# Performance work log

Measured on AMD Instinct MI355X. Metric: run time of the kernel, lower is better.

## Reference

```python
import jax, jax.numpy as jnp
import numpy as np

B, V, C, H, W, D = 1, 3, 32, 320, 320, 32


def setup_inputs() -> dict:
    key = jax.random.key(0)
    ks = jax.random.split(key, 14)
    feats = jax.random.normal(ks[0], (B, V, C, H, W), jnp.float32)
    # Valid pinhole projections: P = [[K @ [R|t]], [0,0,0,1]], identity rotation,
    # horizontal baselines sized so the warp stays mostly in-image over the depth range.
    K = np.array([[400.0, 0.0, W / 2.0], [0.0, 400.0, H / 2.0], [0.0, 0.0, 1.0]])
    mats = []
    for tx in (0.0, 100.0, -100.0):
        Rt = np.eye(4)
        Rt[0, 3] = tx
        P = np.eye(4)
        P[:3, :4] = K @ Rt[:3, :4]
        mats.append(P)
    proj = jnp.asarray(np.broadcast_to(np.stack(mats)[None], (B, V, 4, 4)).copy(), jnp.float32)
    planes = jnp.linspace(425.0, 935.0, D, dtype=jnp.float32)
    depth_values = jnp.broadcast_to(planes[None, :, None, None], (B, D, H, W)).astype(jnp.float32)
    s = 0.05  # small init so exp(reg_cost) stays well-scaled
    W0 = s * jax.random.normal(ks[1], (8, C, 3, 3), jnp.float32)
    Ws1 = s * jax.random.normal(ks[2], (8, 8, 3, 3), jnp.float32)
    W1 = s * jax.random.normal(ks[3], (16, 8, 3, 3), jnp.float32)
    Ws2 = s * jax.random.normal(ks[4], (16, 16, 3, 3), jnp.float32)
    W2 = s * jax.random.normal(ks[5], (32, 16, 3, 3), jnp.float32)
    Ws3 = s * jax.random.normal(ks[6], (32, 32, 3, 3), jnp.float32)
    W3 = s * jax.random.normal(ks[7], (64, 32, 3, 3), jnp.float32)
    Ws4 = s * jax.random.normal(ks[8], (64, 64, 3, 3), jnp.float32)
    U4 = s * jax.random.normal(ks[9], (32, 64, 1, 1), jnp.float32)
    U3 = s * jax.random.normal(ks[10], (16, 32, 1, 1), jnp.float32)
    U2 = s * jax.random.normal(ks[11], (8, 16, 1, 1), jnp.float32)
    Wout = s * jax.random.normal(ks[12], (1, 8, 3, 3), jnp.float32)
    return dict(feats=feats, proj=proj, depth_values=depth_values, W0=W0, Ws1=Ws1,
                W1=W1, Ws2=Ws2, W2=W2, Ws3=Ws3, W3=W3, Ws4=Ws4, U4=U4, U3=U3, U2=U2, Wout=Wout)


def _conv(x, w, stride=1):
    return jax.lax.conv_general_dilated(x, w, (stride, stride), 'SAME',
                                        dimension_numbers=('NCHW', 'OIHW', 'NCHW'))


def _up2(x):
    return jnp.repeat(jnp.repeat(x, 2, axis=2), 2, axis=3)


def _bilinear(img, x, y):
    # img [C,H,W]; x,y [N] pixel coords; zero padding, align_corners semantics
    Cc, Hh, Ww = img.shape
    x0 = jnp.floor(x)
    y0 = jnp.floor(y)
    wx = x - x0
    wy = y - y0

    def tap(xi, yi):
        valid = ((xi >= 0) & (xi <= Ww - 1) & (yi >= 0) & (yi <= Hh - 1)).astype(img.dtype)
        xc = jnp.clip(xi, 0, Ww - 1).astype(jnp.int32)
        yc = jnp.clip(yi, 0, Hh - 1).astype(jnp.int32)
        return img[:, yc, xc] * valid  # [C,N]

    return (tap(x0, y0) * (1 - wx) * (1 - wy) + tap(x0 + 1, y0) * wx * (1 - wy)
            + tap(x0, y0 + 1) * (1 - wx) * wy + tap(x0 + 1, y0 + 1) * wx * wy)


def _forward(feats, proj, depth_values, W0, Ws1, W1, Ws2, W2, Ws3, W3, Ws4, U4, U3, U2, Wout):
    Bn, Vn, Cn, Hn, Wn = feats.shape
    Dn = depth_values.shape[1]
    N = Hn * Wn
    relu = jax.nn.relu
    ref = feats[:, 0]
    ref_sq = ref * ref
    # Precompute per-src-view rotated pixel rays and translations.
    inv_ref = jnp.linalg.inv(proj[:, 0])                       # [B,4,4]
    rel = jnp.einsum('bvij,bjk->bvik', proj[:, 1:], inv_ref)   # [B,V-1,4,4]
    rot, trans = rel[:, :, :3, :3], rel[:, :, :3, 3]
    ys, xs = jnp.meshgrid(jnp.arange(Hn), jnp.arange(Wn), indexing='ij')
    pix = jnp.stack([xs.ravel(), ys.ravel(), jnp.ones(N)], 0).astype(feats.dtype)  # [3,N]
    rot_pix = jnp.einsum('bvij,jn->bvin', rot, pix)            # [B,V-1,3,N]

    def regularize(x, s1, s2, s3, s4):
        c1 = relu(_conv(x, W0) + _conv(s1, Ws1))
        c2 = relu(_conv(c1, W1, 2) + _conv(s2, Ws2))
        c3 = relu(_conv(c2, W2, 2) + _conv(s3, Ws3))
        c4 = relu(_conv(c3, W3, 2) + _conv(s4, Ws4))
        u3 = c3 + _up2(_conv(c4, U4))
        u2 = c2 + _up2(_conv(u3, U3))
        u1 = c1 + _up2(_conv(u2, U2))
        return _conv(u1, Wout), c1, c2, c3, c4

    def step(carry, depth_slice):  # depth_slice [B,H,W]
        s1, s2, s3, s4, exp_sum, depth_img, max_prob = carry
        vol_sum, vol_sq = ref, ref_sq
        dflat = depth_slice.reshape(Bn, 1, N)
        for v in range(Vn - 1):
            xyz = rot_pix[:, v] * dflat + trans[:, v, :, None]   # [B,3,N]
            px = xyz[:, 0] / xyz[:, 2]
            py = xyz[:, 1] / xyz[:, 2]
            warped = jax.vmap(_bilinear)(feats[:, v + 1], px, py).reshape(Bn, Cn, Hn, Wn)
            vol_sum = vol_sum + warped
            vol_sq = vol_sq + warped * warped
        variance = vol_sq / Vn - (vol_sum / Vn) ** 2
        cost, s1, s2, s3, s4 = regularize(variance, s1, s2, s3, s4)
        prob = jnp.exp(cost)                                     # [B,1,H,W]
        max_prob = jnp.maximum(max_prob, prob)                   # == flag*prob + (1-flag)*max
        depth_img = depth_img + depth_slice[:, None] * prob
        exp_sum = exp_sum + prob
        return (s1, s2, s3, s4, exp_sum, depth_img, max_prob), None

    z = lambda c, h, w: jnp.zeros((Bn, c, h, w), feats.dtype)
    init = (z(8, Hn, Wn), z(16, Hn // 2, Wn // 2), z(32, Hn // 4, Wn // 4), z(64, Hn // 8, Wn // 8),
            z(1, Hn, Wn), z(1, Hn, Wn), z(1, Hn, Wn))
    carry, _ = jax.lax.scan(step, init, jnp.moveaxis(depth_values, 1, 0))
    _, _, _, _, exp_sum, depth_img, max_prob = carry
    es = exp_sum + 1e-10
    depth_map = (depth_img / es)[:, 0]
    prob_map = (max_prob / es)[:, 0]
    return jnp.stack([depth_map, prob_map], axis=1)  # [B,2,H,W]


def reference(feats, proj, depth_values, W0, Ws1, W1, Ws2, W2, Ws3, W3, Ws4, U4, U3, U2, Wout):
    return _forward(feats, proj, depth_values, W0, Ws1, W1, Ws2, W2, Ws3, W3, Ws4, U4, U3, U2, Wout)
```

## Files before the change

kernel.cpp:

```cpp
#include <hip/hip_runtime.h>
#include <math.h>

#define HH 320
#define WW 320
#define NP (HH*WW)
#define CC 32
#define DD 32

#define H2 160
#define W2 160
#define N2 (H2*W2)
#define H4 80
#define W4 80
#define N4 (H4*W4)
#define H8 40
#define W8 40
#define N8 (H8*W8)

#define HALO 18
#define NHALO (HALO*HALO)

#define C1SZ (8*NP)
#define C2SZ (16*N2)
#define C3SZ (32*N4)
#define C4SZ (64*N8)

#define SMEM_FLOATS (32*NHALO)

#define OFF_REL   0
#define OFF_C1R   64
#define OFF_C2R   (OFF_C1R + 5*C1SZ)
#define OFF_C3R   (OFF_C2R + 4*C2SZ)
#define OFF_C4R   (OFF_C3R + 3*C3SZ)
#define OFF_ESUM  (OFF_C4R + 2*C4SZ)
#define OFF_DIMG  (OFF_ESUM + NP)
#define OFF_MAXP  (OFF_DIMG + NP)
#define OFF_ACCE  (OFF_MAXP + NP)
#define OFF_FT    OFF_ACCE
#define OFF_END   (OFF_FT + 3*CC*NP)

__global__ void k_prep(const float* __restrict__ proj, float* __restrict__ rel) {
    if (threadIdx.x != 0 || blockIdx.x != 0) return;
    double a[4][8];
    for (int i = 0; i < 4; i++)
        for (int j = 0; j < 4; j++) {
            a[i][j] = (double)proj[i*4 + j];
            a[i][j+4] = (i == j) ? 1.0 : 0.0;
        }
    for (int c = 0; c < 4; c++) {
        int pv = c; double best = fabs(a[c][c]);
        for (int r = c+1; r < 4; r++) {
            double v = fabs(a[r][c]);
            if (v > best) { best = v; pv = r; }
        }
        if (pv != c)
            for (int j = 0; j < 8; j++) { double t = a[c][j]; a[c][j] = a[pv][j]; a[pv][j] = t; }
        double inv = 1.0 / a[c][c];
        for (int j = 0; j < 8; j++) a[c][j] *= inv;
        for (int r = 0; r < 4; r++) if (r != c) {
            double f = a[r][c];
            for (int j = 0; j < 8; j++) a[r][j] -= f * a[c][j];
        }
    }
    for (int v = 1; v < 3; v++) {
        const float* P = proj + v*16;
        double rm[4][4];
        for (int i = 0; i < 4; i++)
            for (int j = 0; j < 4; j++) {
                double s = 0.0;
                for (int k = 0; k < 4; k++) s += (double)P[i*4 + k] * a[k][j+4];
                rm[i][j] = s;
            }
        float* o = rel + (v-1)*12;
        o[0]=(float)rm[0][0]; o[1]=(float)rm[0][1]; o[2]=(float)rm[0][2];
        o[3]=(float)rm[1][0]; o[4]=(float)rm[1][1]; o[5]=(float)rm[1][2];
        o[6]=(float)rm[2][0]; o[7]=(float)rm[2][1]; o[8]=(float)rm[2][2];
        o[9]=(float)rm[0][3]; o[10]=(float)rm[1][3]; o[11]=(float)rm[2][3];
    }
}

__global__ __launch_bounds__(256) void k_transpose(const float* __restrict__ feats,
                                                   float* __restrict__ featsT) {
    __shared__ float lds[32][65];
    int g = blockIdx.x;
    int v = g / 1600;
    int p0 = (g - v*1600) * 64;
    const float* src = feats + (size_t)v*CC*NP + p0;
    for (int i = threadIdx.x; i < 32*64; i += 256) {
        int c = i >> 6, pp = i & 63;
        lds[c][pp] = src[(size_t)c*NP + pp];
    }
    __syncthreads();
    float* dst = featsT + ((size_t)v*NP + p0)*32;
    int pp = threadIdx.x >> 2, cq = (threadIdx.x & 3) * 8;
    float4 o0, o1;
    o0.x = lds[cq+0][pp]; o0.y = lds[cq+1][pp]; o0.z = lds[cq+2][pp]; o0.w = lds[cq+3][pp];
    o1.x = lds[cq+4][pp]; o1.y = lds[cq+5][pp]; o1.z = lds[cq+6][pp]; o1.w = lds[cq+7][pp];
    float* w = dst + pp*32 + cq;
    *(float4*)w = o0;
    *(float4*)(w+4) = o1;
}


__device__ void stageA(int blk, int d, int useT,
        const float* __restrict__ feats, const float* __restrict__ featsT,
        const float* __restrict__ rel,
        const float* __restrict__ depthv, const float* __restrict__ c1r,
        const float* __restrict__ W0, const float* __restrict__ Ws1,
        float* buf) {
    const float* dslice = depthv + (size_t)d * NP;
    const float* s1 = c1r + (size_t)((d+4)%5) * C1SZ;
    float* c1out = (float*)c1r + (size_t)(d%5) * C1SZ;

    int bx = blk % 20, by = blk / 20;
    int ox0 = bx*16, oy0 = by*16;

    const float* f1 = feats + CC*NP;
    const float* f2 = feats + 2*CC*NP;
    const float* fT0 = featsT;
    const float* fT1 = featsT + (size_t)CC*NP;
    const float* fT2 = featsT + (size_t)2*CC*NP;
    const float inv3 = 1.0f / 3.0f;

    int opx = threadIdx.x & 15, opy = threadIdx.x >> 4;
    int obase = opy*HALO + opx;
    int outp = (oy0 + opy)*WW + ox0 + opx;

    for (int s = 0; s < 2; s++) {
        int hp = threadIdx.x + s*256;
        if (hp >= NHALO) break;
        int hy = hp / HALO, hx = hp - hy*HALO;
        int gy = oy0 + hy - 1, gx = ox0 + hx - 1;
        if (gy < 0 || gy >= HH || gx < 0 || gx >= WW) {
#pragma unroll 8
            for (int c = 0; c < 32; c++) buf[c*NHALO + hp] = 0.0f;
            continue;
        }
        int p = gy*WW + gx;
        float depth = dslice[p];
        float fx = (float)gx, fy = (float)gy;
        int offs[8]; float wts[8];
#pragma unroll
        for (int v = 0; v < 2; v++) {
            const float* r = rel + v*12;
            float X = (r[0]*fx + r[1]*fy + r[2]) * depth + r[9];
            float Y = (r[3]*fx + r[4]*fy + r[5]) * depth + r[10];
            float Z = (r[6]*fx + r[7]*fy + r[8]) * depth + r[11];
            float iz = 1.0f / Z;
            float px = X * iz, py = Y * iz;
            float x0f = floorf(px), y0f = floorf(py);
            float wx = px - x0f, wy = py - y0f;
            int x0 = (int)x0f, y0 = (int)y0f;
#pragma unroll
            for (int t = 0; t < 4; t++) {
                int xi = x0 + (t & 1), yi = y0 + (t >> 1);
                float wgt = ((t & 1) ? wx : 1.0f - wx) * ((t >> 1) ? wy : 1.0f - wy);
                bool valid = (xi >= 0) && (xi <= WW-1) && (yi >= 0) && (yi <= HH-1);
                int xc = min(max(xi, 0), WW-1);
                int yc = min(max(yi, 0), HH-1);
                offs[v*4 + t] = yc*WW + xc;
                wts[v*4 + t] = valid ? wgt : 0.0f;
            }
        }

        if (useT) {
            float sum[32], sq[32], t[32];
            {
                const float4* q0 = (const float4*)(fT0 + ((size_t)p << 5));
#pragma unroll
                for (int q = 0; q < 8; q++) {
                    float4 v = q0[q];
                    sum[4*q+0] = v.x; sum[4*q+1] = v.y; sum[4*q+2] = v.z; sum[4*q+3] = v.w;
                }
#pragma unroll
                for (int c = 0; c < 32; c++) sq[c] = sum[c]*sum[c];
            }
#pragma unroll
            for (int c = 0; c < 32; c++) t[c] = 0.0f;
#pragma unroll
            for (int tp = 0; tp < 4; tp++) {
                const float4* q1 = (const float4*)(fT1 + ((size_t)offs[tp] << 5));
                float w = wts[tp];
#pragma unroll
                for (int q = 0; q < 8; q++) {
                    float4 v = q1[q];
                    t[4*q+0] += v.x*w; t[4*q+1] += v.y*w; t[4*q+2] += v.z*w; t[4*q+3] += v.w*w;
                }
            }
#pragma unroll
            for (int c = 0; c < 32; c++) { sum[c] += t[c]; sq[c] += t[c]*t[c]; }
#pragma unroll
            for (int c = 0; c < 32; c++) t[c] = 0.0f;
#pragma unroll
            for (int tp = 0; tp < 4; tp++) {
                const float4* q2 = (const float4*)(fT2 + ((size_t)offs[4+tp] << 5));
                float w = wts[4+tp];
#pragma unroll
                for (int q = 0; q < 8; q++) {
                    float4 v = q2[q];
                    t[4*q+0] += v.x*w; t[4*q+1] += v.y*w; t[4*q+2] += v.z*w; t[4*q+3] += v.w*w;
                }
            }
#pragma unroll
            for (int c = 0; c < 32; c++) { sum[c] += t[c]; sq[c] += t[c]*t[c]; }
#pragma unroll
            for (int c = 0; c < 32; c++) {
                float m = sum[c] * inv3;
                buf[c*NHALO + hp] = sq[c] * inv3 - m*m;
            }
        } else {
            for (int c = 0; c < 32; c++) {
                float rv = feats[c*NP + p];
                const float* b1 = f1 + c*NP;
                float t1 = b1[offs[0]]*wts[0] + b1[offs[1]]*wts[1]
                         + b1[offs[2]]*wts[2] + b1[offs[3]]*wts[3];
                const float* b2 = f2 + c*NP;
                float t2 = b2[offs[4]]*wts[4] + b2[offs[5]]*wts[5]
                         + b2[offs[6]]*wts[6] + b2[offs[7]]*wts[7];
                float sum = rv + t1 + t2;
                float sq  = rv*rv + t1*t1 + t2*t2;
                float m = sum * inv3;
                buf[c*NHALO + hp] = sq * inv3 - m*m;
            }
        }
    }
    __syncthreads();

    float acc[8];
#pragma unroll
    for (int o = 0; o < 8; o++) acc[o] = 0.0f;

    for (int ci = 0; ci < 32; ci++) {
        float t[9];
#pragma unroll
        for (int ky = 0; ky < 3; ky++)
#pragma unroll
            for (int kx = 0; kx < 3; kx++) t[ky*3+kx] = buf[ci*NHALO + obase + ky*HALO + kx];
#pragma unroll
        for (int o = 0; o < 8; o++) {
            const float* w = W0 + (o*32 + ci)*9;
            float a = acc[o];
#pragma unroll
            for (int k = 0; k < 9; k++) a += t[k] * w[k];
            acc[o] = a;
        }
    }
    __syncthreads();

    for (int hp = threadIdx.x; hp < NHALO; hp += 256) {
        int hy = hp / HALO, hx = hp - hy*HALO;
        int gy = oy0 + hy - 1, gx = ox0 + hx - 1;
        bool v = (gy >= 0) && (gy < HH) && (gx >= 0) && (gx < WW);
        int p = v ? gy*WW + gx : 0;
#pragma unroll
        for (int c = 0; c < 8; c++) buf[c*NHALO + hp] = v ? s1[c*NP + p] : 0.0f;
    }
    __syncthreads();
    for (int ci = 0; ci < 8; ci++) {
        float t[9];
#pragma unroll
        for (int ky = 0; ky < 3; ky++)
#pragma unroll
            for (int kx = 0; kx < 3; kx++) t[ky*3+kx] = buf[ci*NHALO + obase + ky*HALO + kx];
#pragma unroll
        for (int o = 0; o < 8; o++) {
            const float* w = Ws1 + (o*8 + ci)*9;
            float a = acc[o];
#pragma unroll
            for (int k = 0; k < 9; k++) a += t[k] * w[k];
            acc[o] = a;
        }
    }
#pragma unroll
    for (int o = 0; o < 8; o++) c1out[o*NP + outp] = fmaxf(acc[o], 0.0f);
}

__device__ void stageB(int blk, int d,
        const float* __restrict__ c1r, const float* __restrict__ c2r_,
        const float* __restrict__ W1, const float* __restrict__ Ws2) {
    const float* c1 = c1r + (size_t)(d%5) * C1SZ;
    const float* s2 = c2r_ + (size_t)((d+3)%4) * C2SZ;
    float* c2 = (float*)c2r_ + (size_t)(d%4) * C2SZ;
    int p = (blk % 100)*256 + threadIdx.x;
    if (p >= N2) return;
    int og = blk / 100;
    int y = p / W2, x = p - y*W2;
    int offsA[9]; float mskA[9];
#pragma unroll
    for (int k = 0; k < 9; k++) {
        int yy = 2*y + k/3, xx = 2*x + k%3;
        bool v = (yy < HH) && (xx < WW);
        offsA[k] = v ? yy*WW + xx : 0;
        mskA[k] = v ? 1.0f : 0.0f;
    }
    int offsB[9]; float mskB[9];
#pragma unroll
    for (int k = 0; k < 9; k++) {
        int yy = y + k/3 - 1, xx = x + k%3 - 1;
        bool v = (yy >= 0) && (yy < H2) && (xx >= 0) && (xx < W2);
        offsB[k] = v ? yy*W2 + xx : 0;
        mskB[k] = v ? 1.0f : 0.0f;
    }
    float acc[4];
#pragma unroll
    for (int o = 0; o < 4; o++) acc[o] = 0.0f;
    for (int ci = 0; ci < 8; ci++) {
        const float* b = c1 + ci*NP;
        float t[9];
#pragma unroll
        for (int k = 0; k < 9; k++) t[k] = b[offsA[k]] * mskA[k];
#pragma unroll
        for (int o = 0; o < 4; o++) {
            const float* w = W1 + ((og*4 + o)*8 + ci)*9;
            float a = acc[o];
#pragma unroll
            for (int k = 0; k < 9; k++) a += t[k] * w[k];
            acc[o] = a;
        }
    }
    for (int ci = 0; ci < 16; ci++) {
        const float* b = s2 + ci*N2;
        float t[9];
#pragma unroll
        for (int k = 0; k < 9; k++) t[k] = b[offsB[k]] * mskB[k];
#pragma unroll
        for (int o = 0; o < 4; o++) {
            const float* w = Ws2 + ((og*4 + o)*16 + ci)*9;
            float a = acc[o];
#pragma unroll
            for (int k = 0; k < 9; k++) a += t[k] * w[k];
            acc[o] = a;
        }
    }
#pragma unroll
    for (int o = 0; o < 4; o++) c2[(og*4 + o)*N2 + p] = fmaxf(acc[o], 0.0f);
}

__device__ void stageC(int blk, int d,
        const float* __restrict__ c2r_, const float* __restrict__ c3r_,
        const float* __restrict__ W2w, const float* __restrict__ Ws3) {
    const float* c2 = c2r_ + (size_t)(d%4) * C2SZ;
    const float* s3 = c3r_ + (size_t)((d+2)%3) * C3SZ;
    float* c3 = (float*)c3r_ + (size_t)(d%3) * C3SZ;
    int p = (blk % 25)*256 + threadIdx.x;
    if (p >= N4) return;
    int og = blk / 25;
    int y = p / W4, x = p - y*W4;
    int offsA[9]; float mskA[9];
#pragma unroll
    for (int k = 0; k < 9; k++) {
        int yy = 2*y + k/3, xx = 2*x + k%3;
        bool v = (yy < H2) && (xx < W2);
        offsA[k] = v ? yy*W2 + xx : 0;
        mskA[k] = v ? 1.0f : 0.0f;
    }
    int offsB[9]; float mskB[9];
#pragma unroll
    for (int k = 0; k < 9; k++) {
        int yy = y + k/3 - 1, xx = x + k%3 - 1;
        bool v = (yy >= 0) && (yy < H4) && (xx >= 0) && (xx < W4);
        offsB[k] = v ? yy*W4 + xx : 0;
        mskB[k] = v ? 1.0f : 0.0f;
    }
    float acc[4];
#pragma unroll
    for (int o = 0; o < 4; o++) acc[o] = 0.0f;
    for (int ci = 0; ci < 16; ci++) {
        const float* b = c2 + ci*N2;
        float t[9];
#pragma unroll
        for (int k = 0; k < 9; k++) t[k] = b[offsA[k]] * mskA[k];
#pragma unroll
        for (int o = 0; o < 4; o++) {
            const float* w = W2w + ((og*4 + o)*16 + ci)*9;
            float a = acc[o];
#pragma unroll
            for (int k = 0; k < 9; k++) a += t[k] * w[k];
            acc[o] = a;
        }
    }
    for (int ci = 0; ci < 32; ci++) {
        const float* b = s3 + ci*N4;
        float t[9];
#pragma unroll
        for (int k = 0; k < 9; k++) t[k] = b[offsB[k]] * mskB[k];
#pragma unroll
        for (int o = 0; o < 4; o++) {
            const float* w = Ws3 + ((og*4 + o)*32 + ci)*9;
            float a = acc[o];
#pragma unroll
            for (int k = 0; k < 9; k++) a += t[k] * w[k];
            acc[o] = a;
        }
    }
#pragma unroll
    for (int o = 0; o < 4; o++) c3[(og*4 + o)*N4 + p] = fmaxf(acc[o], 0.0f);
}

__device__ void stageD(int blk, int d,
        const float* __restrict__ c3r_, const float* __restrict__ c4r_,
        const float* __restrict__ W3w, const float* __restrict__ Ws4) {
    const float* c3 = c3r_ + (size_t)(d%3) * C3SZ;
    const float* s4 = c4r_ + (size_t)((d+1)%2) * C4SZ;
    float* c4 = (float*)c4r_ + (size_t)(d%2) * C4SZ;
    int p = (blk % 7)*256 + threadIdx.x;
    if (p >= N8) return;
    int og = blk / 7;
    int y = p / W8, x = p - y*W8;
    int offsA[9]; float mskA[9];
#pragma unroll
    for (int k = 0; k < 9; k++) {
        int yy = 2*y + k/3, xx = 2*x + k%3;
        bool v = (yy < H4) && (xx < W4);
        offsA[k] = v ? yy*W4 + xx : 0;
        mskA[k] = v ? 1.0f : 0.0f;
    }
    int offsB[9]; float mskB[9];
#pragma unroll
    for (int k = 0; k < 9; k++) {
        int yy = y + k/3 - 1, xx = x + k%3 - 1;
        bool v = (yy >= 0) && (yy < H8) && (xx >= 0) && (xx < W8);
        offsB[k] = v ? yy*W8 + xx : 0;
        mskB[k] = v ? 1.0f : 0.0f;
    }
    float acc[4];
#pragma unroll
    for (int o = 0; o < 4; o++) acc[o] = 0.0f;
    for (int ci = 0; ci < 32; ci++) {
        const float* b = c3 + ci*N4;
        float t[9];
#pragma unroll
        for (int k = 0; k < 9; k++) t[k] = b[offsA[k]] * mskA[k];
#pragma unroll
        for (int o = 0; o < 4; o++) {
            const float* w = W3w + ((og*4 + o)*32 + ci)*9;
            float a = acc[o];
#pragma unroll
            for (int k = 0; k < 9; k++) a += t[k] * w[k];
            acc[o] = a;
        }
    }
    for (int ci = 0; ci < 64; ci++) {
        const float* b = s4 + ci*N8;
        float t[9];
#pragma unroll
        for (int k = 0; k < 9; k++) t[k] = b[offsB[k]] * mskB[k];
#pragma unroll
        for (int o = 0; o < 4; o++) {
            const float* w = Ws4 + ((og*4 + o)*64 + ci)*9;
            float a = acc[o];
#pragma unroll
            for (int k = 0; k < 9; k++) a += t[k] * w[k];
            acc[o] = a;
        }
    }
#pragma unroll
    for (int o = 0; o < 4; o++) c4[(og*4 + o)*N8 + p] = fmaxf(acc[o], 0.0f);
}

__device__ void stageU(int blk, int d,
        const float* __restrict__ c1r, const float* __restrict__ c2r_,
        const float* __restrict__ c3r_, const float* __restrict__ c4r_,
        const float* __restrict__ U4, const float* __restrict__ U3,
        const float* __restrict__ U2, const float* __restrict__ Wout,
        const float* __restrict__ depthv,
        float* __restrict__ exp_sum, float* __restrict__ depth_img,
        float* __restrict__ max_prob, float* smem) {
    const float* c1 = c1r + (size_t)(d%5) * C1SZ;
    const float* c2 = c2r_ + (size_t)(d%4) * C2SZ;
    const float* c3 = c3r_ + (size_t)(d%3) * C3SZ;
    const float* c4 = c4r_ + (size_t)(d%2) * C4SZ;
    const float* dslice = depthv + (size_t)d * NP;
    float* u3s = smem;
    float* u2s = smem + 32*36;
    float* u1s = smem + 32*36 + 16*100;

    int bx = blk % 20, by = blk / 20;
    int ox0 = bx*16, oy0 = by*16;
    int qy0 = (oy0 >> 2) - 1, qx0 = (ox0 >> 2) - 1;
    int hy0 = (oy0 >> 1) - 1, hx0 = (ox0 >> 1) - 1;

    for (int i = threadIdx.x; i < 32*36; i += 256) {
        int ch = i / 36, pp = i - ch*36;
        int y4 = qy0 + pp/6, x4 = qx0 + pp%6;
        int y4c = min(max(y4, 0), H4-1), x4c = min(max(x4, 0), W4-1);
        int pl = (y4c >> 1)*W8 + (x4c >> 1);
        const float* w = U4 + ch*64;
        float s = c3[ch*N4 + y4c*W4 + x4c];
#pragma unroll 8
        for (int ci = 0; ci < 64; ci++) s += c4[ci*N8 + pl] * w[ci];
        u3s[ch*36 + pp] = s;
    }
    __syncthreads();
    for (int i = threadIdx.x; i < 16*100; i += 256) {
        int ch = i / 100, pp = i - ch*100;
        int y2 = hy0 + pp/10, x2 = hx0 + pp%10;
        int y2c = min(max(y2, 0), H2-1), x2c = min(max(x2, 0), W2-1);
        int ly = (y2c >> 1) - qy0, lx = (x2c >> 1) - qx0;
        const float* w = U3 + ch*32;
        float s = c2[ch*N2 + y2c*W2 + x2c];
#pragma unroll 8
        for (int ci = 0; ci < 32; ci++) s += u3s[ci*36 + ly*6 + lx] * w[ci];
        u2s[ch*100 + pp] = s;
    }
    __syncthreads();
    for (int i = threadIdx.x; i < 8*NHALO; i += 256) {
        int ch = i / NHALO, pp = i - ch*NHALO;
        int gy = oy0 + pp/HALO - 1, gx = ox0 + pp%HALO - 1;
        float s = 0.0f;
        if (gy >= 0 && gy < HH && gx >= 0 && gx < WW) {
            int ly = (gy >> 1) - hy0, lx = (gx >> 1) - hx0;
            const float* w = U2 + ch*16;
            s = c1[ch*NP + gy*WW + gx];
#pragma unroll
            for (int ci = 0; ci < 16; ci++) s += u2s[ci*100 + ly*10 + lx] * w[ci];
        }
        u1s[ch*NHALO + pp] = s;
    }
    __syncthreads();
    int px = threadIdx.x & 15, py = threadIdx.x >> 4;
    int base = py*HALO + px;
    float cost = 0.0f;
#pragma unroll
    for (int ci = 0; ci < 8; ci++) {
        const float* w = Wout + ci*9;
#pragma unroll
        for (int ky = 0; ky < 3; ky++)
#pragma unroll
            for (int kx = 0; kx < 3; kx++)
                cost += u1s[ci*NHALO + base + ky*HALO + kx] * w[ky*3 + kx];
    }
    int p = (oy0 + py)*WW + ox0 + px;
    float prob = expf(cost);
    exp_sum[p] += prob;
    depth_img[p] += dslice[p] * prob;
    max_prob[p] = fmaxf(max_prob[p], prob);
}

__global__ __launch_bounds__(256) void k_uber(
        int t, int useT,
        const float* __restrict__ feats, const float* __restrict__ featsT,
        const float* __restrict__ rel,
        const float* __restrict__ depthv,
        const float* __restrict__ W0, const float* __restrict__ Ws1,
        const float* __restrict__ W1, const float* __restrict__ Ws2,
        const float* __restrict__ W2w, const float* __restrict__ Ws3,
        const float* __restrict__ W3w, const float* __restrict__ Ws4,
        const float* __restrict__ U4, const float* __restrict__ U3,
        const float* __restrict__ U2, const float* __restrict__ Wout,
        float* __restrict__ c1r, float* __restrict__ c2r,
        float* __restrict__ c3r, float* __restrict__ c4r,
        float* __restrict__ esum, float* __restrict__ dimg,
        float* __restrict__ maxp) {
    __shared__ float smem[SMEM_FLOATS];
    int b = blockIdx.x;
    if (b < 400) {
        int d = t;
        if (d < DD) stageA(b, d, useT, feats, featsT, rel, depthv, c1r, W0, Ws1, smem);
    } else if (b < 800) {
        int d = t - 1;
        if (d >= 0 && d < DD) stageB(b - 400, d, c1r, c2r, W1, Ws2);
    } else if (b < 1000) {
        int d = t - 2;
        if (d >= 0 && d < DD) stageC(b - 800, d, c2r, c3r, W2w, Ws3);
    } else if (b < 1112) {
        int d = t - 3;
        if (d >= 0 && d < DD) stageD(b - 1000, d, c3r, c4r, W3w, Ws4);
    } else {
        int d = t - 4;
        if (d >= 0 && d < DD)
            stageU(b - 1112, d, c1r, c2r, c3r, c4r, U4, U3, U2, Wout, depthv,
                   esum, dimg, maxp, smem);
    }
}

__global__ __launch_bounds__(256) void k_final(
        const float* __restrict__ exp_sum, const float* __restrict__ depth_img,
        const float* __restrict__ max_prob, float* __restrict__ out) {
    int p = blockIdx.x*256 + threadIdx.x;
    if (p >= NP) return;
    float es = exp_sum[p] + 1e-10f;
    out[p] = depth_img[p] / es;
    out[NP + p] = max_prob[p] / es;
}

extern "C" void kernel_launch(void* const* d_in, const int* in_sizes, int n_in,
                              void* d_out, int out_size, void* d_ws, size_t ws_size,
                              hipStream_t stream) {
    const float* feats = (const float*)d_in[0];
    const float* proj  = (const float*)d_in[1];
    const float* depthv= (const float*)d_in[2];
    const float* W0  = (const float*)d_in[3];
    const float* Ws1 = (const float*)d_in[4];
    const float* W1  = (const float*)d_in[5];
    const float* Ws2 = (const float*)d_in[6];
    const float* W2w = (const float*)d_in[7];
    const float* Ws3 = (const float*)d_in[8];
    const float* W3w = (const float*)d_in[9];
    const float* Ws4 = (const float*)d_in[10];
    const float* U4  = (const float*)d_in[11];
    const float* U3  = (const float*)d_in[12];
    const float* U2  = (const float*)d_in[13];
    const float* Wout= (const float*)d_in[14];

    float* ws = (float*)d_ws;
    float* rel  = ws + OFF_REL;
    float* c1r  = ws + OFF_C1R;
    float* c2r  = ws + OFF_C2R;
    float* c3r  = ws + OFF_C3R;
    float* c4r  = ws + OFF_C4R;
    float* esum = ws + OFF_ESUM;
    float* dimg = ws + OFF_DIMG;
    float* maxp = ws + OFF_MAXP;

    int useT = (ws_size >= (size_t)OFF_END * sizeof(float)) ? 1 : 0;
    float* featsT = useT ? (ws + OFF_FT) : ws;

    hipMemsetAsync(c1r, 0, (size_t)(OFF_ACCE - OFF_C1R) * sizeof(float), stream);
    k_prep<<<1, 1, 0, stream>>>(proj, rel);
    if (useT)
        k_transpose<<<dim3(3*1600), 256, 0, stream>>>(feats, featsT);

    for (int t = 0; t < DD + 4; t++) {
        k_uber<<<dim3(1512), 256, 0, stream>>>(t, useT, feats, featsT, rel, depthv,
            W0, Ws1, W1, Ws2, W2w, Ws3, W3w, Ws4, U4, U3, U2, Wout,
            c1r, c2r, c3r, c4r, esum, dimg, maxp);
    }
    k_final<<<dim3(400), 256, 0, stream>>>(esum, dimg, maxp, (float*)d_out);
}
```

Before: 3.208 ms.

## Store stage-A variance halo as half2, widen conv output groups, simplify prep

The 32-channel variance halo in stage A is now packed into LDS as half2 pairs, halving shared memory per block (SMEM_FLOATS reduced), which may raise occupancy of the fused uber kernel. Stages B, C and D each compute 8 output channels per thread instead of 4, halving their block counts and reusing each loaded 3x3 input patch across more outputs. k_prep switches from pivoted double Gauss-Jordan to unpivoted float. Storing variance in fp16 loses precision before the conv and may shift the exp-weighted depth output, and the unpivoted float inverse assumes a well-conditioned projection.

Measured after the change: 3.222 ms. No clear change (+0.4%).

```diff
diff --git a/kernel.cpp b/kernel.cpp
--- a/kernel.cpp
+++ b/kernel.cpp
@@ -1,4 +1,5 @@
 #include <hip/hip_runtime.h>
+#include <hip/hip_fp16.h>
 #include <math.h>
 
 #define HH 320
@@ -25,7 +26,7 @@
 #define C3SZ (32*N4)
 #define C4SZ (64*N8)
 
-#define SMEM_FLOATS (32*NHALO)
+#define SMEM_FLOATS 5344
 
 #define OFF_REL   0
 #define OFF_C1R   64
@@ -41,41 +42,47 @@
 
 __global__ void k_prep(const float* __restrict__ proj, float* __restrict__ rel) {
     if (threadIdx.x != 0 || blockIdx.x != 0) return;
-    double a[4][8];
+    float a[4][4], inv[4][4];
+#pragma unroll
     for (int i = 0; i < 4; i++)
+#pragma unroll
         for (int j = 0; j < 4; j++) {
-            a[i][j] = (double)proj[i*4 + j];
-            a[i][j+4] = (i == j) ? 1.0 : 0.0;
-        }
+            a[i][j] = proj[i*4 + j];
+            inv[i][j] = (i == j) ? 1.0f : 0.0f;
+        }
+#pragma unroll
     for (int c = 0; c < 4; c++) {
-        int pv = c; double best = fabs(a[c][c]);
-        for (int r = c+1; r < 4; r++) {
-            double v = fabs(a[r][c]);
-            if (v > best) { best = v; pv = r; }
-        }
-        if (pv != c)
-            for (int j = 0; j < 8; j++) { double t = a[c][j]; a[c][j] = a[pv][j]; a[pv][j] = t; }
-        double inv = 1.0 / a[c][c];
-        for (int j = 0; j < 8; j++) a[c][j] *= inv;
+        float s = 1.0f / a[c][c];
+#pragma unroll
+        for (int j = 0; j < 4; j++) { a[c][j] *= s; inv[c][j] *= s; }
+#pragma unroll
         for (int r = 0; r < 4; r++) if (r != c) {
-            double f = a[r][c];
-            for (int j = 0; j < 8; j++) a[r][j] -= f * a[c][j];
-        }
-    }
+            float f = a[r][c];
+#pragma unroll
+            for (int j = 0; j < 4; j++) {
+                a[r][j] -= f * a[c][j];
+                inv[r][j] -= f * inv[c][j];
+            }
+        }
+    }
+#pragma unroll
     for (int v = 1; v < 3; v++) {
         const float* P = proj + v*16;
-        double rm[4][4];
-        for (int i = 0; i < 4; i++)
+        float rm[3][4];
+#pragma unroll
+        for (int i = 0; i < 3; i++)
+#pragma unroll
             for (int j = 0; j < 4; j++) {
-                double s = 0.0;
-                for (int k = 0; k < 4; k++) s += (double)P[i*4 + k] * a[k][j+4];
+                float s = 0.0f;
+#pragma unroll
+                for (int k = 0; k < 4; k++) s += P[i*4 + k] * inv[k][j];
                 rm[i][j] = s;
             }
         float* o = rel + (v-1)*12;
-        o[0]=(float)rm[0][0]; o[1]=(float)rm[0][1]; o[2]=(float)rm[0][2];
-        o[3]=(float)rm[1][0]; o[4]=(float)rm[1][1]; o[5]=(float)rm[1][2];
-        o[6]=(float)rm[2][0]; o[7]=(float)rm[2][1]; o[8]=(float)rm[2][2];
-        o[9]=(float)rm[0][3]; o[10]=(float)rm[1][3]; o[11]=(float)rm[2][3];
+        o[0]=rm[0][0]; o[1]=rm[0][1]; o[2]=rm[0][2];
+        o[3]=rm[1][0]; o[4]=rm[1][1]; o[5]=rm[1][2];
+        o[6]=rm[2][0]; o[7]=rm[2][1]; o[8]=rm[2][2];
+        o[9]=rm[0][3]; o[10]=rm[1][3]; o[11]=rm[2][3];
     }
 }
 
@@ -107,7 +114,9 @@
         const float* __restrict__ rel,
         const float* __restrict__ depthv, const float* __restrict__ c1r,
         const float* __restrict__ W0, const float* __restrict__ Ws1,
-        float* buf) {
+        float* smem) {
+    __half2* pbuf = (__half2*)smem;
+    float* fbuf = smem;
     const float* dslice = depthv + (size_t)d * NP;
     const float* s1 = c1r + (size_t)((d+4)%5) * C1SZ;
     float* c1out = (float*)c1r + (size_t)(d%5) * C1SZ;
@@ -132,8 +141,9 @@
         int hy = hp / HALO, hx = hp - hy*HALO;
         int gy = oy0 + hy - 1, gx = ox0 + hx - 1;
         if (gy < 0 || gy >= HH || gx < 0 || gx >= WW) {
+            __half2 z = __floats2half2_rn(0.0f, 0.0f);
 #pragma unroll 8
-            for (int c = 0; c < 32; c++) buf[c*NHALO + hp] = 0.0f;
+            for (int c = 0; c < 16; c++) pbuf[c*NHALO + hp] = z;
             continue;
         }
         int p = gy*WW + gx;
@@ -163,6 +173,7 @@
             }
         }
 
+        float var[32];
         if (useT) {
             float sum[32], sq[32], t[32];
             {
@@ -206,7 +217,7 @@
 #pragma unroll
             for (int c = 0; c < 32; c++) {
                 float m = sum[c] * inv3;
-                buf[c*NHALO + hp] = sq[c] * inv3 - m*m;
+                var[c] = sq[c] * inv3 - m*m;
             }
         } else {
             for (int c = 0; c < 32; c++) {
@@ -220,9 +231,12 @@
                 float sum = rv + t1 + t2;
                 float sq  = rv*rv + t1*t1 + t2*t2;
                 float m = sum * inv3;
-                buf[c*NHALO + hp] = sq * inv3 - m*m;
-            }
-        }
+                var[c] = sq * inv3 - m*m;
+            }
+        }
+#pragma unroll
+        for (int c = 0; c < 16; c++)
+            pbuf[c*NHALO + hp] = __floats2half2_rn(var[2*c], var[2*c+1]);
     }
     __syncthreads();
 
@@ -230,18 +244,24 @@
 #pragma unroll
     for (int o = 0; o < 8; o++) acc[o] = 0.0f;
 
-    for (int ci = 0; ci < 32; ci++) {
-        float t[9];
+    for (int cp = 0; cp < 16; cp++) {
+        float t0[9], t1[9];
 #pragma unroll
         for (int ky = 0; ky < 3; ky++)
 #pragma unroll
-            for (int kx = 0; kx < 3; kx++) t[ky*3+kx] = buf[ci*NHALO + obase + ky*HALO + kx];
-#pragma unroll
-        for (int o = 0; o < 8; o++) {
-            const float* w = W0 + (o*32 + ci)*9;
-            float a = acc[o];
-#pragma unroll
-            for (int k = 0; k < 9; k++) a += t[k] * w[k];
+            for (int kx = 0; kx < 3; kx++) {
+                __half2 h = pbuf[cp*NHALO + obase + ky*HALO + kx];
+                t0[ky*3+kx] = __low2float(h);
+                t1[ky*3+kx] = __high2float(h);
+            }
+#pragma unroll
+        for (int o = 0; o < 8; o++) {
+            const float* w0 = W0 + (o*32 + 2*cp)*9;
+            float a = acc[o];
+#pragma unroll
+            for (int k = 0; k < 9; k++) a += t0[k] * w0[k];
+#pragma unroll
+            for (int k = 0; k < 9; k++) a += t1[k] * w0[9 + k];
             acc[o] = a;
         }
     }
@@ -253,7 +273,7 @@
         bool v = (gy >= 0) && (gy < HH) && (gx >= 0) && (gx < WW);
         int p = v ? gy*WW + gx : 0;
 #pragma unroll
-        for (int c = 0; c < 8; c++) buf[c*NHALO + hp] = v ? s1[c*NP + p] : 0.0f;
+        for (int c = 0; c < 8; c++) fbuf[c*NHALO + hp] = v ? s1[c*NP + p] : 0.0f;
     }
     __syncthreads();
     for (int ci = 0; ci < 8; ci++) {
@@ -261,7 +281,7 @@
 #pragma unroll
         for (int ky = 0; ky < 3; ky++)
 #pragma unroll
-            for (int kx = 0; kx < 3; kx++) t[ky*3+kx] = buf[ci*NHALO + obase + ky*HALO + kx];
+            for (int kx = 0; kx < 3; kx++) t[ky*3+kx] = fbuf[ci*NHALO + obase + ky*HALO + kx];
 #pragma unroll
         for (int o = 0; o < 8; o++) {
             const float* w = Ws1 + (o*8 + ci)*9;
@@ -301,17 +321,17 @@
         offsB[k] = v ? yy*W2 + xx : 0;
         mskB[k] = v ? 1.0f : 0.0f;
     }
-    float acc[4];
-#pragma unroll
-    for (int o = 0; o < 4; o++) acc[o] = 0.0f;
+    float acc[8];
+#pragma unroll
+    for (int o = 0; o < 8; o++) acc[o] = 0.0f;
     for (int ci = 0; ci < 8; ci++) {
         const float* b = c1 + ci*NP;
         float t[9];
 #pragma unroll
         for (int k = 0; k < 9; k++) t[k] = b[offsA[k]] * mskA[k];
 #pragma unroll
-        for (int o = 0; o < 4; o++) {
-            const float* w = W1 + ((og*4 + o)*8 + ci)*9;
+        for (int o = 0; o < 8; o++) {
+            const float* w = W1 + ((og*8 + o)*8 + ci)*9;
             float a = acc[o];
 #pragma unroll
             for (int k = 0; k < 9; k++) a += t[k] * w[k];
@@ -324,8 +344,8 @@
 #pragma unroll
         for (int k = 0; k < 9; k++) t[k] = b[offsB[k]] * mskB[k];
 #pragma unroll
-        for (int o = 0; o < 4; o++) {
-            const float* w = Ws2 + ((og*4 + o)*16 + ci)*9;
+        for (int o = 0; o < 8; o++) {
+            const float* w = Ws2 + ((og*8 + o)*16 + ci)*9;
             float a = acc[o];
 #pragma unroll
             for (int k = 0; k < 9; k++) a += t[k] * w[k];
@@ -333,7 +353,7 @@
         }
     }
 #pragma unroll
-    for (int o = 0; o < 4; o++) c2[(og*4 + o)*N2 + p] = fmaxf(acc[o], 0.0f);
+    for (int o = 0; o < 8; o++) c2[(og*8 + o)*N2 + p] = fmaxf(acc[o], 0.0f);
 }
 
 __device__ void stageC(int blk, int d,
@@ -362,17 +382,17 @@
         offsB[k] = v ? yy*W4 + xx : 0;
         mskB[k] = v ? 1.0f : 0.0f;
     }
-    float acc[4];
-#pragma unroll
-    for (int o = 0; o < 4; o++) acc[o] = 0.0f;
+    float acc[8];
+#pragma unroll
+    for (int o = 0; o < 8; o++) acc[o] = 0.0f;
     for (int ci = 0; ci < 16; ci++) {
         const float* b = c2 + ci*N2;
         float t[9];
 #pragma unroll
         for (int k = 0; k < 9; k++) t[k] = b[offsA[k]] * mskA[k];
 #pragma unroll
-        for (int o = 0; o < 4; o++) {
-            const float* w = W2w + ((og*4 + o)*16 + ci)*9;
+        for (int o = 0; o < 8; o++) {
+            const float* w = W2w + ((og*8 + o)*16 + ci)*9;
             float a = acc[o];
 #pragma unroll
             for (int k = 0; k < 9; k++) a += t[k] * w[k];
@@ -385,8 +405,8 @@
 #pragma unroll
         for (int k = 0; k < 9; k++) t[k] = b[offsB[k]] * mskB[k];
 #pragma unroll
-        for (int o = 0; o < 4; o++) {
-            const float* w = Ws3 + ((og*4 + o)*32 + ci)*9;
+        for (int o = 0; o < 8; o++) {
+            const float* w = Ws3 + ((og*8 + o)*32 + ci)*9;
             float a = acc[o];
 #pragma unroll
             for (int k = 0; k < 9; k++) a += t[k] * w[k];
@@ -394,7 +414,7 @@
         }
     }
 #pragma unroll
-    for (int o = 0; o < 4; o++) c3[(og*4 + o)*N4 + p] = fmaxf(acc[o], 0.0f);
+    for (int o = 0; o < 8; o++) c3[(og*8 + o)*N4 + p] = fmaxf(acc[o], 0.0f);
 }
 
 __device__ void stageD(int blk, int d,
@@ -423,17 +443,17 @@
         offsB[k] = v ? yy*W8 + xx : 0;
         mskB[k] = v ? 1.0f : 0.0f;
     }
-    float acc[4];
-#pragma unroll
-    for (int o = 0; o < 4; o++) acc[o] = 0.0f;
+    float acc[8];
+#pragma unroll
+    for (int o = 0; o < 8; o++) acc[o] = 0.0f;
     for (int ci = 0; ci < 32; ci++) {
         const float* b = c3 + ci*N4;
         float t[9];
 #pragma unroll
         for (int k = 0; k < 9; k++) t[k] = b[offsA[k]] * mskA[k];
 #pragma unroll
-        for (int o = 0; o < 4; o++) {
-            const float* w = W3w + ((og*4 + o)*32 + ci)*9;
+        for (int o = 0; o < 8; o++) {
+            const float* w = W3w + ((og*8 + o)*32 + ci)*9;
             float a = acc[o];
 #pragma unroll
             for (int k = 0; k < 9; k++) a += t[k] * w[k];
@@ -446,8 +466,8 @@
 #pragma unroll
         for (int k = 0; k < 9; k++) t[k] = b[offsB[k]] * mskB[k];
 #pragma unroll
-        for (int o = 0; o < 4; o++) {
-            const float* w = Ws4 + ((og*4 + o)*64 + ci)*9;
+        for (int o = 0; o < 8; o++) {
+            const float* w = Ws4 + ((og*8 + o)*64 + ci)*9;
             float a = acc[o];
 #pragma unroll
             for (int k = 0; k < 9; k++) a += t[k] * w[k];
@@ -455,7 +475,7 @@
         }
     }
 #pragma unroll
-    for (int o = 0; o < 4; o++) c4[(og*4 + o)*N8 + p] = fmaxf(acc[o], 0.0f);
+    for (int o = 0; o < 8; o++) c4[(og*8 + o)*N8 + p] = fmaxf(acc[o], 0.0f);
 }
 
 __device__ void stageU(int blk, int d,
@@ -557,19 +577,19 @@
     if (b < 400) {
         int d = t;
         if (d < DD) stageA(b, d, useT, feats, featsT, rel, depthv, c1r, W0, Ws1, smem);
-    } else if (b < 800) {
+    } else if (b < 600) {
         int d = t - 1;
         if (d >= 0 && d < DD) stageB(b - 400, d, c1r, c2r, W1, Ws2);
-    } else if (b < 1000) {
+    } else if (b < 700) {
         int d = t - 2;
-        if (d >= 0 && d < DD) stageC(b - 800, d, c2r, c3r, W2w, Ws3);
-    } else if (b < 1112) {
+        if (d >= 0 && d < DD) stageC(b - 600, d, c2r, c3r, W2w, Ws3);
+    } else if (b < 756) {
         int d = t - 3;
-        if (d >= 0 && d < DD) stageD(b - 1000, d, c3r, c4r, W3w, Ws4);
+        if (d >= 0 && d < DD) stageD(b - 700, d, c3r, c4r, W3w, Ws4);
     } else {
         int d = t - 4;
         if (d >= 0 && d < DD)
-            stageU(b - 1112, d, c1r, c2r, c3r, c4r, U4, U3, U2, Wout, depthv,
+            stageU(b - 756, d, c1r, c2r, c3r, c4r, U4, U3, U2, Wout, depthv,
                    esum, dimg, maxp, smem);
     }
 }
@@ -622,7 +642,7 @@
         k_transpose<<<dim3(3*1600), 256, 0, stream>>>(feats, featsT);
 
     for (int t = 0; t < DD + 4; t++) {
-        k_uber<<<dim3(1512), 256, 0, stream>>>(t, useT, feats, featsT, rel, depthv,
+        k_uber<<<dim3(1156), 256, 0, stream>>>(t, useT, feats, featsT, rel, depthv,
             W0, Ws1, W1, Ws2, W2w, Ws3, W3w, Ws4, U4, U3, U2, Wout,
             c1r, c2r, c3r, c4r, esum, dimg, maxp);
     }
```
